# Optimization experiments

Measured on AMD Instinct MI355X. Metric: run time of the kernel, lower is better.

The kernel has to match this reference:

```python
import jax, jax.numpy as jnp
import numpy as np
import math

B, T, D, H = 2, 4096, 1024, 16
DH = D // H
LOCAL = 3
MAX_GATE = 0.6


def dilated_positions(seq_len, local=LOCAL):
    A = local + int(math.ceil(math.log2(max(seq_len, 2)))) + 1
    pos = np.zeros((seq_len, A), np.int32)
    msk = np.zeros((seq_len, A), bool)
    for i in range(seq_len):
        ap = [i] + [i - j for j in range(1, local + 1) if i - j >= 0]
        k = 2
        while 2 ** k <= i:
            ap.append(i - 2 ** k)
            k += 1
        pos[i, :len(ap)] = ap
        msk[i, :len(ap)] = True
    return pos, msk


def pid_proj(x, Wp, Wi, Wd, Wg, bg):
    # x: (B,T,D); W*: (D,D); Wg: (D,3); bg: (3,)
    t = x.shape[1]
    denom = jnp.arange(1, t + 1, dtype=x.dtype)[None, :, None]
    integral = jnp.cumsum(x, axis=1) / denom
    derivative = jnp.concatenate([jnp.zeros_like(x[:, :1]), x[:, 1:] - x[:, :-1]], axis=1)
    g = jax.nn.softmax(x @ Wg + bg, axis=-1)
    g = jnp.minimum(g, MAX_GATE)
    g = g / g.sum(axis=-1, keepdims=True)
    return g[..., 0:1] * (x @ Wp) + g[..., 1:2] * (integral @ Wi) + g[..., 2:3] * (derivative @ Wd)


def setup_inputs() -> dict:
    key = jax.random.key(0)
    ks = jax.random.split(key, 16)
    s = 1.0 / math.sqrt(D)
    inp = {"x": jax.random.normal(ks[0], (B, T, D), jnp.float32)}
    i = 1
    for name in ("q", "k", "v"):
        inp[f"Wp_{name}"] = jax.random.normal(ks[i], (D, D), jnp.float32) * s; i += 1
        inp[f"Wi_{name}"] = jax.random.normal(ks[i], (D, D), jnp.float32) * s * 0.3; i += 1
        inp[f"Wd_{name}"] = jax.random.normal(ks[i], (D, D), jnp.float32) * s * 0.3; i += 1
        inp[f"Wg_{name}"] = jax.random.normal(ks[i], (D, 3), jnp.float32) * s; i += 1
        inp[f"bg_{name}"] = jnp.array([0.5, 0.0, 0.0], jnp.float32)
    inp["Wo"] = jax.random.normal(ks[13], (D, D), jnp.float32) * s
    pos, msk = dilated_positions(T)
    inp["positions"] = jnp.asarray(pos)
    inp["mask"] = jnp.asarray(msk)
    return inp


def reference(x, Wp_q, Wi_q, Wd_q, Wg_q, bg_q,
              Wp_k, Wi_k, Wd_k, Wg_k, bg_k,
              Wp_v, Wi_v, Wd_v, Wg_v, bg_v,
              Wo, positions, mask):
    b, t, d = x.shape
    scale = DH ** -0.5
    def heads(y):  # (B,T,D) -> (B,H,T,DH)
        return y.reshape(b, t, H, DH).transpose(0, 2, 1, 3)
    q = heads(pid_proj(x, Wp_q, Wi_q, Wd_q, Wg_q, bg_q))
    k = heads(pid_proj(x, Wp_k, Wi_k, Wd_k, Wg_k, bg_k))
    v = heads(pid_proj(x, Wp_v, Wi_v, Wd_v, Wg_v, bg_v))
    # gather per-query sparse K/V: (B,H,T,A,DH)
    k_sparse = k[:, :, positions]
    v_sparse = v[:, :, positions]
    scores = jnp.einsum('bhsd,bhsad->bhsa', q, k_sparse) * scale
    scores = jnp.where(mask[None, None], scores, -jnp.inf)
    attn = jax.nn.softmax(scores, axis=-1)
    out = jnp.einsum('bhsa,bhsad->bhsd', attn, v_sparse)
    out = out.transpose(0, 2, 1, 3).reshape(b, t, d)
    return out @ Wo
```

## Files before the change

### kernel.cpp

```cpp
#include <hip/hip_runtime.h>
#include <hip/hip_bf16.h>
#include <cstdint>

#define B_   2
#define T_   4096
#define D_   1024
#define H_   16
#define DH_  64
#define M_   (B_*T_)
#define K3_  (3*D_)
#define TC_  32
#define NCH_ (T_/TC_)

typedef __attribute__((ext_vector_type(4))) float  f32x4;
typedef __attribute__((ext_vector_type(8))) short  short8;

__device__ __forceinline__ float bf2f(ushort u) {
    union { uint32_t i; float f; } v; v.i = ((uint32_t)u) << 16; return v.f;
}
__device__ __forceinline__ ushort f2bf(float f) {
    union { float f; uint32_t i; } v; v.f = f;
    uint32_t r = v.i + 0x7FFF + ((v.i >> 16) & 1);
    return (ushort)(r >> 16);
}

template<bool F32>
__device__ __forceinline__ float ld_in(const void* p, size_t i) {
    if (F32) return ((const float*)p)[i];
    return bf2f(((const ushort*)p)[i]);
}
template<bool F32>
__device__ __forceinline__ void ld4_in(const void* p, size_t i, float* o) {
    if (F32) {
        float4 v = *(const float4*)((const float*)p + i);
        o[0] = v.x; o[1] = v.y; o[2] = v.z; o[3] = v.w;
    } else {
        ushort4 v = *(const ushort4*)((const ushort*)p + i);
        o[0] = bf2f(v.x); o[1] = bf2f(v.y); o[2] = bf2f(v.z); o[3] = bf2f(v.w);
    }
}

__device__ __forceinline__ void st_c(ushort* p, float v) { *p = f2bf(v); }
__device__ __forceinline__ void st_c(float*  p, float v) { *p = v; }

#define GLOAD_LDS16(g, l) \
    __builtin_amdgcn_global_load_lds((const __attribute__((address_space(1))) void*)(g), \
                                     (__attribute__((address_space(3))) void*)(l), 16, 0, 0)

__global__ void detect_kernel(const ushort* __restrict__ xu, int* __restrict__ flag) {
    __shared__ int cnt;
    if (threadIdx.x == 0) cnt = 0;
    __syncthreads();
    int c = 0;
    for (int i = threadIdx.x; i < 16384; i += 256) {
        ushort u = xu[i];
        if ((u & 0x7F80) == 0x7F80) c++;
    }
    if (c) atomicAdd(&cnt, c);
    __syncthreads();
    if (threadIdx.x == 0) flag[0] = (cnt > 0) ? 1 : 0;
}

template<bool F32>
__device__ __forceinline__ void gates_body(const void* x,
                                           const void* Wg_q, const void* bg_q,
                                           const void* Wg_k, const void* bg_k,
                                           const void* Wg_v, const void* bg_v,
                                           float* __restrict__ g9) {
    const int wave = threadIdx.x >> 6, lane = threadIdx.x & 63;
    const int row  = blockIdx.x * 4 + wave;
    const size_t xoff = (size_t)row * D_;
    float acc[9] = {0,0,0,0,0,0,0,0,0};
    for (int d0 = lane * 4; d0 < D_; d0 += 256) {
        float xv[4], wq[12], wk[12], wv[12];
        ld4_in<F32>(x, xoff + d0, xv);
        #pragma unroll
        for (int q = 0; q < 3; q++) {
            ld4_in<F32>(Wg_q, (size_t)d0*3 + q*4, wq + q*4);
            ld4_in<F32>(Wg_k, (size_t)d0*3 + q*4, wk + q*4);
            ld4_in<F32>(Wg_v, (size_t)d0*3 + q*4, wv + q*4);
        }
        #pragma unroll
        for (int e = 0; e < 4; e++)
            #pragma unroll
            for (int c = 0; c < 3; c++) {
                acc[0+c] += xv[e] * wq[e*3+c];
                acc[3+c] += xv[e] * wk[e*3+c];
                acc[6+c] += xv[e] * wv[e*3+c];
            }
    }
    #pragma unroll
    for (int i = 0; i < 9; i++) {
        #pragma unroll
        for (int o = 32; o >= 1; o >>= 1) acc[i] += __shfl_xor(acc[i], o, 64);
    }
    const void* bgs[3] = {bg_q, bg_k, bg_v};
    float g[9];
    #pragma unroll
    for (int p = 0; p < 3; p++) {
        float l0 = acc[p*3+0] + ld_in<F32>(bgs[p], 0);
        float l1 = acc[p*3+1] + ld_in<F32>(bgs[p], 1);
        float l2 = acc[p*3+2] + ld_in<F32>(bgs[p], 2);
        float mx = fmaxf(l0, fmaxf(l1, l2));
        float e0 = expf(l0-mx), e1 = expf(l1-mx), e2 = expf(l2-mx);
        float s  = e0+e1+e2;
        float g0 = fminf(e0/s, 0.6f), g1 = fminf(e1/s, 0.6f), g2 = fminf(e2/s, 0.6f);
        float s2 = g0+g1+g2;
        g0 /= s2; g1 /= s2; g2 /= s2;
        float g1c = fmaxf(g1, 1e-30f), g2c = fmaxf(g2, 1e-30f);
        g[p*3+0] = g0 / g1c;
        g[p*3+1] = g1c / g2c;
        g[p*3+2] = g2c;
    }
    if (lane == 0) {
        #pragma unroll
        for (int i = 0; i < 9; i++) g9[(size_t)row*9 + i] = g[i];
    }
}
__global__ void gates_kernel(const void* x,
                             const void* Wg_q, const void* bg_q,
                             const void* Wg_k, const void* bg_k,
                             const void* Wg_v, const void* bg_v,
                             const int* __restrict__ flag, float* __restrict__ g9) {
    if (flag[0]) gates_body<true >(x, Wg_q, bg_q, Wg_k, bg_k, Wg_v, bg_v, g9);
    else         gates_body<false>(x, Wg_q, bg_q, Wg_k, bg_k, Wg_v, bg_v, g9);
}

template<bool F32>
__device__ __forceinline__ void chunk_sum_body(const void* x, float* __restrict__ part) {
    const int d = blockIdx.x * 256 + threadIdx.x;
    const int tc = blockIdx.y, b = blockIdx.z;
    const size_t base = ((size_t)b*T_ + (size_t)tc*TC_) * D_ + d;
    float s = 0.f;
    for (int i = 0; i < TC_; i++) s += ld_in<F32>(x, base + (size_t)i * D_);
    part[((size_t)b*NCH_ + tc) * D_ + d] = s;
}
__global__ void chunk_sum_kernel(const void* x, const int* __restrict__ flag,
                                 float* __restrict__ part) {
    if (flag[0]) chunk_sum_body<true >(x, part);
    else         chunk_sum_body<false>(x, part);
}

__global__ void scan_part_kernel(float* __restrict__ part) {
    const int idx = blockIdx.x * 64 + threadIdx.x;
    const int b = idx >> 10, d = idx & (D_-1);
    float run = 0.f;
    for (int tc = 0; tc < NCH_; tc++) {
        size_t o = ((size_t)b*NCH_ + tc) * D_ + d;
        float v = part[o]; part[o] = run; run += v;
    }
}

template<bool F32>
__device__ __forceinline__ void build_xs_body(const void* x, const float* __restrict__ part,
                                              ushort* __restrict__ Xc) {
    const int d0 = threadIdx.x * 4;
    const int tc = blockIdx.y, b = blockIdx.z;
    const int t0 = tc * TC_;
    float carry[4], prev[4];
    {
        float4 c4 = *(const float4*)&part[((size_t)b*NCH_ + tc) * D_ + d0];
        carry[0] = c4.x; carry[1] = c4.y; carry[2] = c4.z; carry[3] = c4.w;
    }
    const size_t xbase = ((size_t)b*T_ + t0) * D_ + d0;
    if (t0 > 0) ld4_in<F32>(x, xbase - D_, prev);
    else        { prev[0] = prev[1] = prev[2] = prev[3] = 0.f; }
    for (int i = 0; i < TC_; i++) {
        const int t = t0 + i;
        float xv[4];
        ld4_in<F32>(x, xbase + (size_t)i * D_, xv);
        const float rinv = 1.0f / (float)(t + 1);
        ushort4 ox, oi, od;
        {
            carry[0] += xv[0]; carry[1] += xv[1]; carry[2] += xv[2]; carry[3] += xv[3];
            ox = make_ushort4(f2bf(xv[0]), f2bf(xv[1]), f2bf(xv[2]), f2bf(xv[3]));
            oi = make_ushort4(f2bf(carry[0]*rinv), f2bf(carry[1]*rinv),
                              f2bf(carry[2]*rinv), f2bf(carry[3]*rinv));
            if (t == 0) od = make_ushort4(0, 0, 0, 0);
            else od = make_ushort4(f2bf(xv[0]-prev[0]), f2bf(xv[1]-prev[1]),
                                   f2bf(xv[2]-prev[2]), f2bf(xv[3]-prev[3]));
            prev[0] = xv[0]; prev[1] = xv[1]; prev[2] = xv[2]; prev[3] = xv[3];
        }
        const size_t base = ((size_t)b*T_ + t) * K3_ + d0;
        *(ushort4*)(Xc + base       ) = ox;
        *(ushort4*)(Xc + base +   D_) = oi;
        *(ushort4*)(Xc + base + 2*D_) = od;
    }
}
__global__ void build_xs_kernel(const void* x, const float* __restrict__ part,
                                const int* __restrict__ flag, ushort* __restrict__ Xc) {
    if (flag[0]) build_xs_body<true >(x, part, Xc);
    else         build_xs_body<false>(x, part, Xc);
}

struct WPtrs { const void* w[10]; };
template<bool F32>
__device__ __forceinline__ void transpose_w_body(WPtrs ptrs, ushort* __restrict__ Wt,
                                                 ushort* __restrict__ WoT) {
    const int z = blockIdx.z;
    const void* src = ptrs.w[z];
    __shared__ float tile[32][33];
    const int tx = threadIdx.x & 31, ty = threadIdx.x >> 5;
    const int d0 = blockIdx.x * 32, c0 = blockIdx.y * 32;
    #pragma unroll
    for (int i = 0; i < 4; i++) {
        int r = ty + i*8;
        tile[r][tx] = ld_in<F32>(src, (size_t)(d0 + r) * D_ + c0 + tx);
    }
    __syncthreads();
    if (z < 9) {
        const int p = z / 3, j = z % 3;
        #pragma unroll
        for (int i = 0; i < 4; i++) {
            int r = ty + i*8;
            Wt[(size_t)(p*D_ + c0 + r) * K3_ + j*D_ + d0 + tx] = f2bf(tile[tx][r]);
        }
    } else {
        #pragma unroll
        for (int i = 0; i < 4; i++) {
            int r = ty + i*8;
            WoT[(size_t)(c0 + r) * D_ + d0 + tx] = f2bf(tile[tx][r]);
        }
    }
}
__global__ void transpose_w_kernel(WPtrs ptrs, const int* __restrict__ flag,
                                   ushort* __restrict__ Wt, ushort* __restrict__ WoT) {
    if (flag[0]) transpose_w_body<true >(ptrs, Wt, WoT);
    else         transpose_w_body<false>(ptrs, Wt, WoT);
}

template<typename CT, int NTILES, bool GATED>
__global__ __launch_bounds__(512, 2) void gemm_bt8_kernel(
        const ushort* __restrict__ Abase,
        const ushort* __restrict__ Bt,
        CT* __restrict__ C,
        const float* __restrict__ g9,
        int K, int lda, int ldc) {
    __shared__ __align__(16) ushort LDS[3 * 24576];
    const int tid  = threadIdx.x;
    const int lane = tid & 63;
    const int wave = tid >> 6;
    const int wm   = wave >> 2;
    const int wn   = wave & 3;
    const int quad = lane >> 4, l16 = lane & 15, sw = l16 & 7;

    const int MT     = M_ / 128;
    const int cpx    = (MT * NTILES) / 8;
    const int wg     = (blockIdx.x % 8) * cpx + blockIdx.x / 8;
    const int mchunk = MT / 8;
    const int rem    = wg % (mchunk * NTILES);
    const int mt     = (wg / (mchunk * NTILES)) * mchunk + (rem % mchunk);
    const int nt     = rem / mchunk;
    const int m0 = mt * 128;
    const int n0 = nt * 256;
    const int p  = n0 >> 10;

    const ushort* asrc[2]; int aoff[2];
    #pragma unroll
    for (int g = 0; g < 2; g++) {
        const int I = g*512 + tid;
        const int row = I >> 3, c8 = (I & 7) ^ (row & 7);
        asrc[g] = Abase + (size_t)(m0 + row) * lda + c8*8;
        aoff[g] = I * 8;
    }
    const ushort* bsrc[4]; int boff[4];
    #pragma unroll
    for (int g = 0; g < 4; g++) {
        const int I = g*512 + tid;
        const int row = I >> 3, c8 = (I & 7) ^ (row & 7);
        bsrc[g] = Bt + (size_t)(n0 + row) * K + c8*8;
        boff[g] = I * 8;
    }
    int ard[4], brd[4];
    #pragma unroll
    for (int i = 0; i < 4; i++) {
        ard[i] = (wm*64 + i*16 + l16) * 64;
        brd[i] = (wn*64 + i*16 + l16) * 64;
    }

    const int NKT = K >> 6;
    f32x4 acc[4][4] = {};

    #pragma unroll
    for (int g = 0; g < 2; g++) GLOAD_LDS16(asrc[g], &LDS[aoff[g]]);
    #pragma unroll
    for (int g = 0; g < 4; g++) GLOAD_LDS16(bsrc[g], &LDS[8192 + boff[g]]);
    #pragma unroll
    for (int g = 0; g < 2; g++) GLOAD_LDS16(asrc[g] + 64, &LDS[24576 + aoff[g]]);
    #pragma unroll
    for (int g = 0; g < 4; g++) GLOAD_LDS16(bsrc[g] + 64, &LDS[24576 + 8192 + boff[g]]);
    asm volatile("s_waitcnt vmcnt(6)" ::: "memory");
    __builtin_amdgcn_s_barrier();

    for (int t = 0; t < NKT; ++t) {
        const int cur = t % 3;
        const int ab  = cur * 24576;
        const int bb  = ab + 8192;
        const bool do_stage = (t + 2 < NKT);
        const int sb  = ((t + 2) % 3) * 24576;
        const int skt = (t + 2) << 6;

        short8 af[4], bfr[4];

        #pragma unroll
        for (int i = 0; i < 4; i++)
            af[i]  = *(const short8*)&LDS[ab + ard[i] + (quad ^ sw) * 8];
        #pragma unroll
        for (int j = 0; j < 4; j++)
            bfr[j] = *(const short8*)&LDS[bb + brd[j] + (quad ^ sw) * 8];
        if (do_stage) {
            GLOAD_LDS16(asrc[0] + skt, &LDS[sb + aoff[0]]);
            GLOAD_LDS16(asrc[1] + skt, &LDS[sb + aoff[1]]);
            GLOAD_LDS16(bsrc[0] + skt, &LDS[sb + 8192 + boff[0]]);
        }
        __builtin_amdgcn_s_barrier();
        asm volatile("s_waitcnt lgkmcnt(0)" ::: "memory");
        __builtin_amdgcn_sched_barrier(0);
        __builtin_amdgcn_s_setprio(1);
        #pragma unroll
        for (int i = 0; i < 4; i++)
            #pragma unroll
            for (int j = 0; j < 4; j++)
                acc[i][j] = __builtin_amdgcn_mfma_f32_16x16x32_bf16(af[i], bfr[j], acc[i][j], 0, 0, 0);
        __builtin_amdgcn_s_setprio(0);
        __builtin_amdgcn_s_barrier();

        #pragma unroll
        for (int i = 0; i < 4; i++)
            af[i]  = *(const short8*)&LDS[ab + ard[i] + ((quad + 4) ^ sw) * 8];
        #pragma unroll
        for (int j = 0; j < 4; j++)
            bfr[j] = *(const short8*)&LDS[bb + brd[j] + ((quad + 4) ^ sw) * 8];
        if (do_stage) {
            GLOAD_LDS16(bsrc[1] + skt, &LDS[sb + 8192 + boff[1]]);
            GLOAD_LDS16(bsrc[2] + skt, &LDS[sb + 8192 + boff[2]]);
            GLOAD_LDS16(bsrc[3] + skt, &LDS[sb + 8192 + boff[3]]);
        }
        __builtin_amdgcn_s_barrier();
        asm volatile("s_waitcnt lgkmcnt(0)" ::: "memory");
        __builtin_amdgcn_sched_barrier(0);
        __builtin_amdgcn_s_setprio(1);
        #pragma unroll
        for (int i = 0; i < 4; i++)
            #pragma unroll
            for (int j = 0; j < 4; j++)
                acc[i][j] = __builtin_amdgcn_mfma_f32_16x16x32_bf16(af[i], bfr[j], acc[i][j], 0, 0, 0);
        __builtin_amdgcn_s_setprio(0);
        if (do_stage)          asm volatile("s_waitcnt vmcnt(6)" ::: "memory");
        else if (t + 1 < NKT)  asm volatile("s_waitcnt vmcnt(0)" ::: "memory");
        __builtin_amdgcn_s_barrier();

        if (GATED && ((t & 15) == 15)) {
            const int seg = t >> 4;
            #pragma unroll
            for (int i = 0; i < 4; i++) {
                float gv[4];
                #pragma unroll
                for (int rg = 0; rg < 4; rg++) {
                    const int rrow = m0 + wm*64 + i*16 + quad*4 + rg;
                    gv[rg] = g9[(size_t)rrow * 9 + p*3 + seg];
                }
                #pragma unroll
                for (int j = 0; j < 4; j++)
                    #pragma unroll
                    for (int rg = 0; rg < 4; rg++)
                        acc[i][j][rg] *= gv[rg];
            }
        }
    }

    #pragma unroll
    for (int i = 0; i < 4; i++) {
        #pragma unroll
        for (int j = 0; j < 4; j++) {
            const int rrow = m0 + wm*64 + i*16 + quad*4;
            const int col  = n0 + wn*64 + j*16 + l16;
            #pragma unroll
            for (int rg = 0; rg < 4; rg++)
                st_c(&C[(size_t)(rrow + rg) * ldc + col], acc[i][j][rg]);
        }
    }
}

__global__ __launch_bounds__(128) void attn_kernel(const ushort* __restrict__ QKV,
                                                   ushort* __restrict__ AO) {
    const int tid = threadIdx.x;
    const int bi  = blockIdx.x;
    const int bt  = (bi & 7) * 1024 + (bi >> 3);
    const int t   = bt & (T_-1);
    const size_t qrow = (size_t)bt * K3_;
    const int e0 = tid * 8;

    const short8 q8 = *(const short8*)(QKV + qrow + e0);
    float qf[8];
    #pragma unroll
    for (int j = 0; j < 8; j++) qf[j] = bf2f((ushort)q8[j]);

    float sc[14];
    #pragma unroll
    for (int a = 0; a < 14; a++) {
        const int off = (a <= 3) ? a : (1 << (a - 2));
        float pv = -1e30f;
        if (off <= t) {
            const short8 k8 = *(const short8*)(QKV + qrow - (size_t)off*K3_ + D_ + e0);
            float pp = 0.f;
            #pragma unroll
            for (int j = 0; j < 8; j++) pp += qf[j] * bf2f((ushort)k8[j]);
            pp += __shfl_xor(pp, 1, 64);
            pp += __shfl_xor(pp, 2, 64);
            pp += __shfl_xor(pp, 4, 64);
            pv = pp * 0.125f;
        }
        sc[a] = pv;
    }
    float mx = -1e30f;
    #pragma unroll
    for (int a = 0; a < 14; a++) mx = fmaxf(mx, sc[a]);
    float ev[14], s = 0.0f;
    #pragma unroll
    for (int a = 0; a < 14; a++) { ev[a] = (sc[a] > -1e29f) ? expf(sc[a] - mx) : 0.0f; s += ev[a]; }
    const float rs = 1.0f / s;

    float ao[8] = {0,0,0,0,0,0,0,0};
    #pragma unroll
    for (int a = 0; a < 14; a++) {
        const int off = (a <= 3) ? a : (1 << (a - 2));
        if (off <= t) {
            const short8 v8 = *(const short8*)(QKV + qrow - (size_t)off*K3_ + 2*D_ + e0);
            const float w = ev[a] * rs;
            #pragma unroll
            for (int j = 0; j < 8; j++) ao[j] += w * bf2f((ushort)v8[j]);
        }
    }
    short8 o8;
    #pragma unroll
    for (int j = 0; j < 8; j++) o8[j] = (short)f2bf(ao[j]);
    *(short8*)(AO + (size_t)bt * D_ + e0) = o8;
}

extern "C" void kernel_launch(void* const* d_in, const int* in_sizes, int n_in,
                              void* d_out, int out_size, void* d_ws, size_t ws_size,
                              hipStream_t stream) {
    (void)in_sizes; (void)n_in; (void)out_size; (void)ws_size;
    const void* x    = d_in[0];
    const void* Wg_q = d_in[4];  const void* bg_q = d_in[5];
    const void* Wg_k = d_in[9];  const void* bg_k = d_in[10];
    const void* Wg_v = d_in[14]; const void* bg_v = d_in[15];

    char* ws = (char*)d_ws;
    int*    flag = (int*)ws;    ws += 16;
    float*  g9   = (float*)ws;  ws += (size_t)M_*9*4;
    float*  part = (float*)ws;  ws += (size_t)B_*NCH_*D_*4;
    ushort* Wt   = (ushort*)ws; ws += (size_t)K3_*K3_*2;
    ushort* WoT  = (ushort*)ws; ws += (size_t)D_*D_*2;
    ushort* Xc   = (ushort*)ws; ws += (size_t)M_*K3_*2;
    ushort* QKV  = (ushort*)ws; ws += (size_t)M_*K3_*2;
    ushort* AO   = (ushort*)ws; ws += (size_t)M_*D_*2;

    detect_kernel<<<1, 256, 0, stream>>>((const ushort*)x, flag);
    gates_kernel<<<M_/4, 256, 0, stream>>>(x, Wg_q, bg_q, Wg_k, bg_k, Wg_v, bg_v, flag, g9);
    chunk_sum_kernel<<<dim3(D_/256, NCH_, B_), 256, 0, stream>>>(x, flag, part);
    scan_part_kernel<<<32, 64, 0, stream>>>(part);
    WPtrs wp;
    wp.w[0] = d_in[1];  wp.w[1] = d_in[2];  wp.w[2] = d_in[3];
    wp.w[3] = d_in[6];  wp.w[4] = d_in[7];  wp.w[5] = d_in[8];
    wp.w[6] = d_in[11]; wp.w[7] = d_in[12]; wp.w[8] = d_in[13];
    wp.w[9] = d_in[16];
    transpose_w_kernel<<<dim3(32, 32, 10), 256, 0, stream>>>(wp, flag, Wt, WoT);
    build_xs_kernel<<<dim3(1, NCH_, B_), 256, 0, stream>>>(x, part, flag, Xc);
    gemm_bt8_kernel<ushort, 12, true><<<768, 512, 0, stream>>>(Xc, Wt, QKV, g9, K3_, K3_, K3_);
    attn_kernel<<<B_*T_, 128, 0, stream>>>(QKV, AO);
    gemm_bt8_kernel<float, 4, false><<<256, 512, 0, stream>>>(AO, WoT, (float*)d_out, nullptr, D_, D_, D_);
}
```

Baseline: 439.5 us.

## Replace QKV GEMM with 128x128-tile 4-wave double-buffered kernel

Adds a new gated GEMM kernel for the QKV projection. It uses 128x128 output tiles, 256 threads (4 waves, each computing 64x64), and two LDS buffers. The old kernel used 8 waves and three buffers. The grid doubles to 1536 blocks, which aims for better occupancy and tail balance on the large projection. The trade-offs are less operand reuse per block and more global traffic for A and B tiles.

```diff
diff --git a/kernel.cpp b/kernel.cpp
--- a/kernel.cpp
+++ b/kernel.cpp
@@ -229,6 +229,141 @@
     else         transpose_w_body<false>(ptrs, Wt, WoT);
 }
 
+template<int NTILES>
+__global__ __launch_bounds__(256, 2) void gemm_bt4_kernel(
+        const ushort* __restrict__ Abase,
+        const ushort* __restrict__ Bt,
+        ushort* __restrict__ C,
+        const float* __restrict__ g9) {
+    __shared__ __align__(16) ushort LDS[2 * 16384];
+    const int tid  = threadIdx.x;
+    const int lane = tid & 63;
+    const int wave = tid >> 6;
+    const int wm   = wave >> 1;
+    const int wn   = wave & 1;
+    const int quad = lane >> 4, l16 = lane & 15, sw = l16 & 7;
+
+    const int MT     = M_ / 128;
+    const int cpx    = (MT * NTILES) / 8;
+    const int wg     = (blockIdx.x % 8) * cpx + blockIdx.x / 8;
+    const int rem    = wg % (8 * NTILES);
+    const int mt     = (wg / (8 * NTILES)) * 8 + (rem & 7);
+    const int nt     = rem >> 3;
+    const int m0 = mt * 128;
+    const int n0 = nt * 128;
+    const int p  = n0 >> 10;
+
+    const ushort* asrc[4]; const ushort* bsrc[4]; int goff[4];
+    #pragma unroll
+    for (int g = 0; g < 4; g++) {
+        const int I = g*256 + tid;
+        const int row = I >> 3, c8 = (I & 7) ^ (row & 7);
+        asrc[g] = Abase + (size_t)(m0 + row) * K3_ + c8*8;
+        bsrc[g] = Bt    + (size_t)(n0 + row) * K3_ + c8*8;
+        goff[g] = I * 8;
+    }
+    int ard[4], brd[4];
+    #pragma unroll
+    for (int i = 0; i < 4; i++) {
+        ard[i] = (wm*64 + i*16 + l16) * 64;
+        brd[i] = 8192 + (wn*64 + i*16 + l16) * 64;
+    }
+
+    constexpr int NKT = K3_ >> 6;
+    f32x4 acc[4][4] = {};
+
+    #pragma unroll
+    for (int g = 0; g < 4; g++) GLOAD_LDS16(asrc[g], &LDS[goff[g]]);
+    #pragma unroll
+    for (int g = 0; g < 4; g++) GLOAD_LDS16(bsrc[g], &LDS[8192 + goff[g]]);
+    asm volatile("s_waitcnt vmcnt(0)" ::: "memory");
+    __builtin_amdgcn_s_barrier();
+
+    for (int t = 0; t < NKT; ++t) {
+        const int bb = (t & 1) << 14;
+        const int sb = bb ^ 16384;
+        const int skt = (t + 1) << 6;
+        const bool stage = (t + 1 < NKT);
+
+        short8 af[4], bfr[4];
+
+        #pragma unroll
+        for (int i = 0; i < 4; i++)
+            af[i]  = *(const short8*)&LDS[bb + ard[i] + (quad ^ sw) * 8];
+        #pragma unroll
+        for (int j = 0; j < 4; j++)
+            bfr[j] = *(const short8*)&LDS[bb + brd[j] + (quad ^ sw) * 8];
+        if (stage) {
+            #pragma unroll
+            for (int g = 0; g < 4; g++) GLOAD_LDS16(asrc[g] + skt, &LDS[sb + goff[g]]);
+        }
+        __builtin_amdgcn_s_barrier();
+        asm volatile("s_waitcnt lgkmcnt(0)" ::: "memory");
+        __builtin_amdgcn_sched_barrier(0);
+        __builtin_amdgcn_s_setprio(1);
+        #pragma unroll
+        for (int i = 0; i < 4; i++)
+            #pragma unroll
+            for (int j = 0; j < 4; j++)
+                acc[i][j] = __builtin_amdgcn_mfma_f32_16x16x32_bf16(af[i], bfr[j], acc[i][j], 0, 0, 0);
+        __builtin_amdgcn_s_setprio(0);
+        __builtin_amdgcn_s_barrier();
+
+        #pragma unroll
+        for (int i = 0; i < 4; i++)
+            af[i]  = *(const short8*)&LDS[bb + ard[i] + ((quad + 4) ^ sw) * 8];
+        #pragma unroll
+        for (int j = 0; j < 4; j++)
+            bfr[j] = *(const short8*)&LDS[bb + brd[j] + ((quad + 4) ^ sw) * 8];
+        if (stage) {
+            #pragma unroll
+            for (int g = 0; g < 4; g++) GLOAD_LDS16(bsrc[g] + skt, &LDS[sb + 8192 + goff[g]]);
+        }
+        __builtin_amdgcn_s_barrier();
+        asm volatile("s_waitcnt lgkmcnt(0)" ::: "memory");
+        __builtin_amdgcn_sched_barrier(0);
+        __builtin_amdgcn_s_setprio(1);
+        #pragma unroll
+        for (int i = 0; i < 4; i++)
+            #pragma unroll
+            for (int j = 0; j < 4; j++)
+                acc[i][j] = __builtin_amdgcn_mfma_f32_16x16x32_bf16(af[i], bfr[j], acc[i][j], 0, 0, 0);
+        __builtin_amdgcn_s_setprio(0);
+        if (stage) asm volatile("s_waitcnt vmcnt(0)" ::: "memory");
+        __builtin_amdgcn_s_barrier();
+
+        if ((t & 15) == 15) {
+            const int seg = t >> 4;
+            #pragma unroll
+            for (int i = 0; i < 4; i++) {
+                float gv[4];
+                #pragma unroll
+                for (int rg = 0; rg < 4; rg++) {
+                    const int rrow = m0 + wm*64 + i*16 + quad*4 + rg;
+                    gv[rg] = g9[(size_t)rrow * 9 + p*3 + seg];
+                }
+                #pragma unroll
+                for (int j = 0; j < 4; j++)
+                    #pragma unroll
+                    for (int rg = 0; rg < 4; rg++)
+                        acc[i][j][rg] *= gv[rg];
+            }
+        }
+    }
+
+    #pragma unroll
+    for (int i = 0; i < 4; i++) {
+        #pragma unroll
+        for (int j = 0; j < 4; j++) {
+            const int rrow = m0 + wm*64 + i*16 + quad*4;
+            const int col  = n0 + wn*64 + j*16 + l16;
+            #pragma unroll
+            for (int rg = 0; rg < 4; rg++)
+                C[(size_t)(rrow + rg) * K3_ + col] = f2bf(acc[i][j][rg]);
+        }
+    }
+}
+
 template<typename CT, int NTILES, bool GATED>
 __global__ __launch_bounds__(512, 2) void gemm_bt8_kernel(
         const ushort* __restrict__ Abase,
@@ -468,7 +603,7 @@
     wp.w[9] = d_in[16];
     transpose_w_kernel<<<dim3(32, 32, 10), 256, 0, stream>>>(wp, flag, Wt, WoT);
     build_xs_kernel<<<dim3(1, NCH_, B_), 256, 0, stream>>>(x, part, flag, Xc);
-    gemm_bt8_kernel<ushort, 12, true><<<768, 512, 0, stream>>>(Xc, Wt, QKV, g9, K3_, K3_, K3_);
+    gemm_bt4_kernel<24><<<1536, 256, 0, stream>>>(Xc, Wt, QKV, g9);
     attn_kernel<<<B_*T_, 128, 0, stream>>>(QKV, AO);
     gemm_bt8_kernel<float, 4, false><<<256, 512, 0, stream>>>(AO, WoT, (float*)d_out, nullptr, D_, D_, D_);
 }
```

Result: slower. 462.5 us (+5.2%).
